# Kernel tuning notes

Measured on AMD Instinct MI355X. Metric: run time of the kernel, lower is better.

Reference implementation:

```python
import jax, jax.numpy as jnp
import numpy as np
import math

B, L, D, P, H, WIN, MAXLEN = 2, 2048, 256, 32, 4, 5, 16384


def setup_inputs() -> dict:
    key = jax.random.key(0)
    ks = iter(jax.random.split(key, 40))
    def w(shape, scale=0.05):
        return jax.random.normal(next(ks), shape, jnp.float32) * scale
    inp = {
        'x': jax.random.normal(next(ks), (B, L, D), jnp.float32),
        'pos_phases': jax.random.normal(next(ks), (MAXLEN, P), jnp.float32) * math.pi,
        # mem1_content_encoder
        'w_content': w((D, D)), 'b_content': jnp.zeros((D,), jnp.float32),
        # head_offset_predictors (stacked over H): Linear(D+P, D//2) -> GELU -> Linear(D//2, P+1)
        'hop_w1': w((H, D // 2, D + P)), 'hop_b1': jnp.zeros((H, D // 2), jnp.float32),
        'hop_w2': w((H, P + 1, D // 2)), 'hop_b2': jnp.zeros((H, P + 1), jnp.float32),
        # content_phase_encoder
        'w_cpe': w((P, D)), 'b_cpe': jnp.zeros((P,), jnp.float32),
        # value_encoder
        'w_val': w((D, D)), 'b_val': jnp.zeros((D,), jnp.float32),
        # kv_context_encoder
        'w_ctx': w((D, D)), 'b_ctx': jnp.zeros((D,), jnp.float32),
        # kv_storage_key: Linear(2D, D) -> GELU -> Linear(D, P)
        'kv_w1': w((D, 2 * D)), 'kv_b1': jnp.zeros((D,), jnp.float32),
        'kv_w2': w((P, D)), 'kv_b2': jnp.zeros((P,), jnp.float32),
        # store_gate: Linear(D, D//2) -> GELU -> Linear(D//2, 1) -> Sigmoid
        'sg_w1': w((D // 2, D)), 'sg_b1': jnp.zeros((D // 2,), jnp.float32),
        'sg_w2': w((1, D // 2)), 'sg_b2': jnp.zeros((1,), jnp.float32),
        # to_out: LayerNorm(D) -> Linear(D, D)
        'ln_g': jnp.ones((D,), jnp.float32), 'ln_b': jnp.zeros((D,), jnp.float32),
        'w_out': w((D, D)), 'b_out': jnp.zeros((D,), jnp.float32),
    }
    return inp


def reference(x, pos_phases, w_content, b_content, hop_w1, hop_b1, hop_w2, hop_b2,
              w_cpe, b_cpe, w_val, b_val, w_ctx, b_ctx, kv_w1, kv_b1, kv_w2, kv_b2,
              sg_w1, sg_b1, sg_w2, sg_b2, ln_g, ln_b, w_out, b_out):
    gelu = lambda t: jax.nn.gelu(t, approximate=False)  # torch exact GELU
    pp = pos_phases[:L]                      # (L,P)
    pos_cos, pos_sin = jnp.cos(pp), jnp.sin(pp)

    # ---- phasor memory 1: position-bound content cumsum ----
    content = x @ w_content.T + b_content    # (B,L,D)
    mem1_cos = jnp.cumsum(pos_cos[None, :, :, None] * content[:, :, None, :], axis=1)  # (B,L,P,D)
    mem1_sin = jnp.cumsum(pos_sin[None, :, :, None] * content[:, :, None, :], axis=1)

    # ---- per-head learned offsets ----
    offset_input = jnp.concatenate([x, jnp.broadcast_to(pp[None], (B, L, P))], axis=-1)  # (B,L,D+P)
    h1 = gelu(jnp.einsum('blf,hgf->bhlg', offset_input, hop_w1) + hop_b1[None, :, None, :])
    off = jnp.einsum('bhlg,hpg->bhlp', h1, hop_w2) + hop_b2[None, :, None, :]  # (B,H,L,P+1)
    center = jnp.tanh(off[..., :P]) * math.pi    # (B,H,L,P)
    ww = jax.nn.sigmoid(off[..., P:]) * 2 + 0.1  # (B,H,L,1)

    head_ret = jnp.zeros((B, H, L, D), x.dtype)
    tot_w = jnp.zeros((B, H, L, 1), x.dtype)
    half = WIN // 2
    for delta in range(-half, half + 1):
        wgt = jnp.exp(-0.5 * delta ** 2 / (ww ** 2 + 1e-6))
        op = center + delta * 0.1
        oc, os = jnp.cos(op), jnp.sin(op)
        qc = pos_cos[None, None] * oc - pos_sin[None, None] * os
        qs = pos_sin[None, None] * oc + pos_cos[None, None] * os
        ret = (jnp.einsum('blpd,bhlp->bhld', mem1_cos, qc)
               + jnp.einsum('blpd,bhlp->bhld', mem1_sin, qs)) / math.sqrt(P)
        head_ret = head_ret + wgt * ret
        tot_w = tot_w + wgt
    multi_head_out = (head_ret / (tot_w + 1e-6)).mean(axis=1)  # (B,L,D)

    # ---- kv phasor memory ----
    key_ph = jnp.tanh(x @ w_cpe.T + b_cpe) * math.pi            # (B,L,P)
    values = x @ w_val.T + b_val                                 # (B,L,D)
    store_gate = jax.nn.sigmoid(gelu(x @ sg_w1.T + sg_b1) @ sg_w2.T + sg_b2)  # (B,L,1)
    ctx = x @ w_ctx.T + b_ctx
    ctx_avg = jnp.cumsum(ctx, axis=1) / jnp.arange(1, L + 1, dtype=x.dtype)[None, :, None]
    storage_in = jnp.concatenate([x, ctx_avg], axis=-1)          # (B,L,2D)
    sp = jnp.tanh(gelu(storage_in @ kv_w1.T + kv_b1) @ kv_w2.T + kv_b2) * math.pi  # (B,L,P)
    gated_v = values * store_gate                                # (B,L,D)
    kv_cos = jnp.cumsum(jnp.cos(sp)[..., None] * gated_v[:, :, None, :], axis=1)  # (B,L,P,D)
    kv_sin = jnp.cumsum(jnp.sin(sp)[..., None] * gated_v[:, :, None, :], axis=1)
    gate_cum = jnp.clip(jnp.cumsum(store_gate, axis=1), 1.0, None)  # (B,L,1)
    kv_ret = (jnp.einsum('blpd,blp->bld', kv_cos, jnp.cos(key_ph))
              + jnp.einsum('blpd,blp->bld', kv_sin, jnp.sin(key_ph)))
    kv_ret = kv_ret / (jnp.sqrt(gate_cum) * math.sqrt(P))

    # ---- output projection ----
    combined = multi_head_out + kv_ret
    mu = combined.mean(-1, keepdims=True)
    var = combined.var(-1, keepdims=True)
    ln = (combined - mu) / jnp.sqrt(var + 1e-5) * ln_g + ln_b
    return x + ln @ w_out.T + b_out
```

## Files before the change

### kernel.cpp

```cpp
#include <hip/hip_runtime.h>
#include <hip/hip_bf16.h>

#define BB 2
#define LL 2048
#define DD 256
#define PP 32
#define PX 64
#define NROW (BB*LL)
#define COLS 1440
#define KIN 288
#define CC 64
#define NC (LL/CC)
#define PI_F 3.14159265358979323846f

typedef __attribute__((ext_vector_type(8))) short bf16x8;
typedef __attribute__((ext_vector_type(4))) float f32x4;

__device__ __forceinline__ float gelu_f(float v){
    return 0.5f*v*(1.0f+erff(v*0.70710678118654752440f));
}
__device__ __forceinline__ float sigm_f(float v){
    return 1.0f/(1.0f+expf(-v));
}
__device__ __forceinline__ short f2b(float v){
    __hip_bfloat16 h = __float2bfloat16(v);
    return *reinterpret_cast<short*>(&h);
}
__device__ __forceinline__ float b2f(unsigned short u){
    unsigned int x = ((unsigned int)u)<<16;
    return __uint_as_float(x);
}

__global__ void kprep(const float* w_content,const float* w_val,const float* w_ctx,
                      const float* w_cpe,const float* sg_w1,const float* hop_w1,
                      const float* b_content,const float* b_val,const float* b_ctx,
                      const float* b_cpe,const float* sg_b1,const float* hop_b1,
                      const float* pos_phases,const float* kv_w1,const float* kv_w2,
                      const float* hop_w2,const float* w_out,const float* x,
                      short* W_catb,float* bias_cat,float* w2mem,
                      short* kvw1b,short* kvw2b,float* hop_w2T,short* w_outb,
                      short* Xb,short* Xin2b){
    int idx = blockIdx.x*256 + threadIdx.x;
    int n1 = COLS*KIN;
    if (idx < n1){
        int row = idx / KIN, k = idx % KIN;
        float v = 0.f;
        if      (row < 256){ if (k<256) v = w_content[row*256+k]; }
        else if (row < 512){ if (k<256) v = w_val[(row-256)*256+k]; }
        else if (row < 768){ if (k<256) v = w_ctx[(row-512)*256+k]; }
        else if (row < 800){ if (k<256) v = w_cpe[(row-768)*256+k]; }
        else if (row < 928){ if (k<256) v = sg_w1[(row-800)*256+k]; }
        else               { v = hop_w1[(row-928)*288 + k]; }
        W_catb[idx] = f2b(v);
        return;
    }
    idx -= n1;
    if (idx < COLS){
        int row = idx; float v = 0.f;
        if      (row < 256) v = b_content[row];
        else if (row < 512) v = b_val[row-256];
        else if (row < 768) v = b_ctx[row-512];
        else if (row < 800) v = b_cpe[row-768];
        else if (row < 928) v = sg_b1[row-800];
        else                v = hop_b1[row-928];
        bias_cat[row] = v;
        return;
    }
    idx -= COLS;
    if (idx < LL*PP){
        int l = idx/PP, p = idx%PP;
        float ph = pos_phases[l*PP+p];
        w2mem[l*PX+p]     = cosf(ph);
        w2mem[l*PX+32+p]  = sinf(ph);
        return;
    }
    idx -= LL*PP;
    if (idx < 256*512){ kvw1b[idx] = f2b(kv_w1[idx]); return; }
    idx -= 256*512;
    if (idx < 32*256){ kvw2b[idx] = f2b(kv_w2[idx]); return; }
    idx -= 32*256;
    if (idx < 128*132){
        int k=idx/132, o=idx%132;
        hop_w2T[idx] = hop_w2[o*128+k];
        return;
    }
    idx -= 128*132;
    if (idx < 256*256){ w_outb[idx] = f2b(w_out[idx]); return; }
    idx -= 256*256;
    if (idx < NROW*KIN){
        int r = idx / KIN, d = idx % KIN;
        float v;
        if (d < 256){ v = x[(size_t)r*DD + d]; Xin2b[(size_t)r*512 + d] = f2b(v); }
        else          v = pos_phases[(r % LL)*PP + (d-256)];
        Xb[idx] = f2b(v);
    }
}

__global__ __launch_bounds__(256) void kA_gemm(const short* Xb,const short* Wb,short* Yb){
    int t=threadIdx.x;
    int wid=t>>6, l=t&63;
    int q=blockIdx.x;
    int ct=q%15, rt=q/15;
    int r0=rt*64 + wid*16;
    int c0=ct*96;
    int lr=l&15, lk=(l>>4)*8;
    const short* ap = Xb + (size_t)(r0+lr)*KIN + lk;
    const short* bp = Wb + (size_t)(c0+lr)*KIN + lk;
    f32x4 acc[6];
    #pragma unroll
    for (int f=0;f<6;f++) acc[f]=(f32x4){0.f,0.f,0.f,0.f};
    for (int ks=0;ks<9;ks++){
        bf16x8 a = *(const bf16x8*)(ap + ks*32);
        #pragma unroll
        for (int f=0;f<6;f++){
            bf16x8 b = *(const bf16x8*)(bp + (size_t)f*16*KIN + ks*32);
            acc[f] = __builtin_amdgcn_mfma_f32_16x16x32_bf16(a,b,acc[f],0,0,0);
        }
    }
    int orow = r0 + (l>>4)*4;
    int ocol = c0 + lr;
    #pragma unroll
    for (int f=0;f<6;f++){
        #pragma unroll
        for (int qq=0;qq<4;qq++){
            Yb[(size_t)(orow+qq)*COLS + ocol + 16*f] = f2b(acc[f][qq]);
        }
    }
}

__global__ __launch_bounds__(256,4) void kA_post(const short* Yb,const float* bias_cat,
        const float* sg_w2,const float* sg_b2,
        const float* hop_w2T,const float* hop_b2,const float* pos_phases,
        short* contentb,short* gatedvb,float* ctx,float* key_ph,
        float* store_gate,float* coef_mem){
    __shared__ float yb[4][1448];
    __shared__ float red[4][32];
    __shared__ float offb[4][136];
    __shared__ float scl[4][4];
    __shared__ float sgvv[4];
    int t=threadIdx.x;
    int r0=blockIdx.x*4;
    {
        const ushort4* Yu4 = (const ushort4*)(Yb) + (size_t)r0*360;
        #pragma unroll
        for (int i=0;i<6;i++){
            int chunk=i*256+t;
            if (chunk<1440){
                int r=chunk/360, c=(chunk%360)*4;
                ushort4 s4 = Yu4[chunk];
                float4 bc = *(const float4*)&bias_cat[c];
                yb[r][c+0]=b2f(s4.x)+bc.x;
                yb[r][c+1]=b2f(s4.y)+bc.y;
                yb[r][c+2]=b2f(s4.z)+bc.z;
                yb[r][c+3]=b2f(s4.w)+bc.w;
            }
        }
    }
    __syncthreads();
    #pragma unroll
    for (int r=0;r<4;r++){
        contentb[(size_t)(r0+r)*DD+t] = f2b(yb[r][t]);
        ctx[(size_t)(r0+r)*DD+t]      = yb[r][512+t];
    }
    #pragma unroll
    for (int j=0;j<8;j++){
        int idx=j*256+t, r=idx>>9, g=idx&511;
        yb[r][928+g] = gelu_f(yb[r][928+g]);
    }
    if (t<128){
        int r=t>>5, j=t&31;
        float s=0.f;
        #pragma unroll
        for (int k=0;k<4;k++){
            int jj=j+32*k;
            s += gelu_f(yb[r][800+jj])*sg_w2[jj];
        }
        red[r][j]=s;
        key_ph[(size_t)(r0+r)*PP+j] = tanhf(yb[r][768+j])*PI_F;
    }
    __syncthreads();
    if (t<128){
        int r=t>>5;
        float s=red[r][t&31];
        #pragma unroll
        for (int off=16;off>=1;off>>=1) s += __shfl_down(s,off,32);
        if ((t&31)==0){
            float g=sigm_f(s+sg_b2[0]);
            sgvv[r]=g;
            store_gate[r0+r]=g;
        }
    }
    for (int sIdx=t; sIdx<528; sIdx+=256){
        int r=sIdx/132, o=sIdx%132, h=o/33;
        const float* yh=&yb[r][928+h*128];
        float a0=0.f,a1=0.f,a2=0.f,a3=0.f;
        #pragma unroll 8
        for (int k=0;k<128;k+=4){
            a0 += hop_w2T[(size_t)(k+0)*132+o]*yh[k+0];
            a1 += hop_w2T[(size_t)(k+1)*132+o]*yh[k+1];
            a2 += hop_w2T[(size_t)(k+2)*132+o]*yh[k+2];
            a3 += hop_w2T[(size_t)(k+3)*132+o]*yh[k+3];
        }
        offb[r][o]=a0+a1+a2+a3+hop_b2[o];
    }
    __syncthreads();
    #pragma unroll
    for (int r=0;r<4;r++) gatedvb[(size_t)(r0+r)*DD+t]=f2b(yb[r][256+t]*sgvv[r]);
    if (t<16){
        int r=t>>2, h=t&3;
        const float c01=0.99500416527802576610f;
        const float c02=0.98006657784124163112f;
        float ww=sigm_f(offb[r][h*33+32])*2.0f+0.1f;
        float iw=1.0f/(ww*ww+1e-6f);
        float w1=expf(-0.5f*iw);
        float w2=expf(-2.0f*iw);
        float tot=1.0f+2.0f*w1+2.0f*w2;
        float Wc =1.0f+2.0f*w1*c01+2.0f*w2*c02;
        scl[r][h]=Wc/((tot+1e-6f)*5.65685424949238019520f*4.0f);
    }
    __syncthreads();
    if (t<128){
        int r=t>>5, p=t&31;
        int l=(r0+r)%LL;
        float ppv=pos_phases[l*PP+p];
        float ca=0.f, sb=0.f;
        #pragma unroll
        for (int h=0;h<4;h++){
            float center=tanhf(offb[r][h*33+p])*PI_F;
            float ang=ppv+center;
            float sc=scl[r][h];
            ca+=sc*cosf(ang);
            sb+=sc*sinf(ang);
        }
        coef_mem[(size_t)(r0+r)*PX+p]=ca;
        coef_mem[(size_t)(r0+r)*PX+32+p]=sb;
    }
}

__global__ void k3a_ctxsum(const float* ctx,float* ctxcs){
    int t=threadIdx.x;
    int bi=blockIdx.x;
    int c=bi%NC, b=bi/NC;
    float s=0.f;
    for (int i=0;i<CC;i++) s += ctx[((size_t)b*LL + c*CC + i)*DD + t];
    ctxcs[(size_t)(b*NC+c)*DD + t] = s;
}
__global__ void k3c_ctxavg(const float* ctx,const float* ctxcs,short* Xin2b){
    int t=threadIdx.x;
    int bi=blockIdx.x;
    int c=bi%NC, b=bi/NC;
    float run=0.f;
    for (int cc=0;cc<c;cc++) run += ctxcs[(size_t)(b*NC+cc)*DD+t];
    for (int i=0;i<CC;i++){
        int l = c*CC+i;
        run += ctx[((size_t)b*LL+l)*DD + t];
        Xin2b[((size_t)b*LL+l)*512 + 256 + t] = f2b(run/(float)(l+1));
    }
}

__global__ __launch_bounds__(256) void kmid(const short* Xin2b,const short* kvw1b,
        const float* kv_b1, short* Hb,
        const float* store_gate,const float* key_ph,float* coefkv){
    __shared__ float sh[2048];
    __shared__ float red[256];
    __shared__ float rsgS[64];
    int t=threadIdx.x;
    if (blockIdx.x < 256){
        int wid=t>>6, l=t&63;
        int q=blockIdx.x;
        int nt=q&3, mt=q>>2;
        int r0=mt*64 + wid*16;
        int c0=nt*64;
        int lr=l&15, lk=(l>>4)*8;
        const short* ap = Xin2b + (size_t)(r0+lr)*512 + lk;
        const short* bp = kvw1b + (size_t)(c0+lr)*512 + lk;
        f32x4 acc[4];
        #pragma unroll
        for (int f=0;f<4;f++) acc[f]=(f32x4){0.f,0.f,0.f,0.f};
        for (int ks=0;ks<16;ks++){
            bf16x8 a = *(const bf16x8*)(ap + ks*32);
            #pragma unroll
            for (int f=0;f<4;f++){
                bf16x8 b = *(const bf16x8*)(bp + (size_t)f*16*512 + ks*32);
                acc[f] = __builtin_amdgcn_mfma_f32_16x16x32_bf16(a,b,acc[f],0,0,0);
            }
        }
        int orow = r0 + (l>>4)*4;
        #pragma unroll
        for (int f=0;f<4;f++){
            int oc = c0 + lr + 16*f;
            float bias = kv_b1[oc];
            #pragma unroll
            for (int qq=0;qq<4;qq++){
                Hb[(size_t)(orow+qq)*256 + oc] = f2b(gelu_f(acc[f][qq]+bias));
            }
        }
        return;
    }
    int q=blockIdx.x-256;
    int c=q&31, b=q>>5;
    int n=(c+1)*CC;
    for (int i=t;i<n;i+=256) sh[i]=store_gate[(size_t)b*LL+i];
    __syncthreads();
    float p=0.f;
    for (int i=t;i<c*CC;i+=256) p+=sh[i];
    red[t]=p;
    __syncthreads();
    for (int off=128;off>=1;off>>=1){
        if (t<off) red[t]+=red[t+off];
        __syncthreads();
    }
    float S0=red[0];
    if (t<64){
        float s=sh[c*CC+t];
        #pragma unroll
        for (int off=1;off<64;off<<=1){
            float v=__shfl_up(s,off);
            if (t>=off) s+=v;
        }
        rsgS[t]=rsqrtf(fmaxf(S0+s,1.0f)*32.0f);
    }
    __syncthreads();
    #pragma unroll
    for (int j=0;j<8;j++){
        int g2=t+j*256;
        int l=g2>>5, pp=g2&31;
        float a=key_ph[((size_t)b*LL + c*CC + l)*PP + pp];
        float rv=rsgS[l];
        coefkv[((size_t)b*LL + c*CC + l)*PX + pp]      = cosf(a)*rv;
        coefkv[((size_t)b*LL + c*CC + l)*PX + 32 + pp] = sinf(a)*rv;
    }
}

__global__ __launch_bounds__(256) void k3d2(const short* Hb,const short* kvw2b,
        const float* kv_b2, float* w2kv){
    int t=threadIdx.x;
    int wid=t>>6, l=t&63;
    int mt=blockIdx.x;
    int r0=mt*64 + wid*16;
    int lr=l&15, lk=(l>>4)*8;
    const short* ap = Hb + (size_t)(r0+lr)*256 + lk;
    const short* bp = kvw2b + (size_t)lr*256 + lk;
    f32x4 acc0=(f32x4){0.f,0.f,0.f,0.f};
    f32x4 acc1=(f32x4){0.f,0.f,0.f,0.f};
    for (int ks=0;ks<8;ks++){
        bf16x8 a  = *(const bf16x8*)(ap + ks*32);
        bf16x8 b0 = *(const bf16x8*)(bp + ks*32);
        bf16x8 b1 = *(const bf16x8*)(bp + (size_t)16*256 + ks*32);
        acc0 = __builtin_amdgcn_mfma_f32_16x16x32_bf16(a,b0,acc0,0,0,0);
        acc1 = __builtin_amdgcn_mfma_f32_16x16x32_bf16(a,b1,acc1,0,0,0);
    }
    int orow=r0+(l>>4)*4;
    #pragma unroll
    for (int f=0;f<2;f++){
        int p = lr + 16*f;
        float bias = kv_b2[p];
        f32x4 av = f? acc1:acc0;
        #pragma unroll
        for (int qq=0;qq<4;qq++){
            float sp=tanhf(av[qq]+bias)*PI_F;
            w2kv[(size_t)(orow+qq)*PX + p]    = cosf(sp);
            w2kv[(size_t)(orow+qq)*PX + 32+p] = sinf(sp);
        }
    }
}

__global__ __launch_bounds__(256) void k4_chunksum(
        const short* valA,const float* w2A,int w2bA,
        const short* valB,const float* w2B,int w2bB,
        float* CS){
    __shared__ float w2s[CC][PX];
    int t=threadIdx.x, q=blockIdx.x;
    int dq=q&3, c=(q>>2)&31, b=(q>>7)&1, inst=q>>8;
    const short* val = inst? valB:valA;
    const float* w2  = inst? w2B:w2A;
    int w2b          = inst? w2bB:w2bA;
    for (int i=0;i<16;i++){
        int idx=i*256+t;
        int l=idx>>6, p=idx&63;
        w2s[l][p]=w2[(size_t)w2b*b + (size_t)(c*CC+l)*PX + p];
    }
    __syncthreads();
    int d=t&63, pg=t>>6;
    float acc[16];
    #pragma unroll
    for (int j=0;j<16;j++) acc[j]=0.f;
    const short* vp = val + ((size_t)b*LL + c*CC)*DD + dq*64 + d;
    for (int l=0;l<CC;l++){
        float v = b2f((unsigned short)vp[(size_t)l*DD]);
        const float4* wr=(const float4*)&w2s[l][pg*16];
        #pragma unroll
        for (int k=0;k<4;k++){
            float4 w=wr[k];
            acc[4*k]   += w.x*v;
            acc[4*k+1] += w.y*v;
            acc[4*k+2] += w.z*v;
            acc[4*k+3] += w.w*v;
        }
    }
    float* cp = CS + (((size_t)(inst*BB+b)*NC + c)*PX + pg*16)*DD + dq*64 + d;
    #pragma unroll
    for (int j=0;j<16;j++) cp[(size_t)j*DD]=acc[j];
}

__global__ void k5_prefix(float* CS){
    int g=blockIdx.x*256+threadIdx.x;
    int d=g&255, p2=(g>>8)&63, b=(g>>14)&1, inst=g>>15;
    size_t base=(((size_t)(inst*BB+b)*NC)*PX+p2)*DD+d;
    float v[NC];
    #pragma unroll
    for (int c=0;c<NC;c++) v[c]=CS[base+(size_t)c*PX*DD];
    float run=0.f;
    #pragma unroll
    for (int c=0;c<NC;c++){
        float tmp=v[c];
        CS[base+(size_t)c*PX*DD]=run;
        run+=tmp;
    }
}

__global__ __launch_bounds__(256) void k6_attn(
        const float* coefA,const float* w2A,int w2bA,const short* valA,float* outA,
        const float* coefB,const float* w2B,int w2bB,const short* valB,float* outB,
        const float* CS){
    __shared__ float coefs[CC][PX+1];
    __shared__ float w2s[CC][PX];
    __shared__ float S[CC][CC+1];
    int t=threadIdx.x, q=blockIdx.x;
    int dq=q&3, qc=(q>>2)&31, b=(q>>7)&1, inst=q>>8;
    const float* coef = inst? coefB:coefA;
    const float* w2   = inst? w2B:w2A;
    int w2b           = inst? w2bB:w2bA;
    const short* val  = inst? valB:valA;
    float* out        = inst? outB:outA;
    int d0 = dq*64;
    for (int i=0;i<16;i++){
        int idx=i*256+t;
        int l=idx>>6, p=idx&63;
        coefs[l][p]=coef[((size_t)b*LL + qc*CC + l)*PX + p];
        w2s[l][p]  =w2[(size_t)w2b*b + (size_t)(qc*CC+l)*PX + p];
    }
    __syncthreads();
    {
        int l=t&63, lpb=(t>>6)*16;
        float cf[PX];
        #pragma unroll
        for (int p=0;p<PX;p++) cf[p]=coefs[l][p];
        for (int qq=0;qq<16;qq++){
            int lp=lpb+qq;
            float s=0.f;
            if (lp<=l){
                const float4* wr=(const float4*)&w2s[lp][0];
                #pragma unroll
                for (int k=0;k<16;k++){
                    float4 w=wr[k];
                    s += w.x*cf[4*k]+w.y*cf[4*k+1]+w.z*cf[4*k+2]+w.w*cf[4*k+3];
                }
            }
            S[l][lp]=s;
        }
    }
    __syncthreads();
    {
        int d=t&63, lq=t>>6;
        float acc[16];
        #pragma unroll
        for (int i=0;i<16;i++) acc[i]=0.f;
        const float* pfx = CS + (((size_t)(inst*BB+b)*NC + qc)*PX)*DD + d0 + d;
        for (int p=0;p<PX;p++){
            float pf = pfx[(size_t)p*DD];
            #pragma unroll
            for (int i=0;i<16;i++) acc[i] += coefs[lq*16+i][p]*pf;
        }
        const short* vptr = val + ((size_t)b*LL + qc*CC)*DD + d0 + d;
        int kmax = lq*16+16;
        for (int lp=0; lp<kmax; lp++){
            float v = b2f((unsigned short)vptr[(size_t)lp*DD]);
            #pragma unroll
            for (int i=0;i<16;i++) acc[i] += S[lq*16+i][lp]*v;
        }
        float* op = out + ((size_t)b*LL + qc*CC + lq*16)*DD + d0 + d;
        #pragma unroll
        for (int i=0;i<16;i++) op[(size_t)i*DD] = acc[i];
    }
}

__global__ __launch_bounds__(256) void k7_final(const float* comb,const float* kvout,
        const float* x,const float* ln_g,const float* ln_b,const short* w_outb,const float* b_out,
        float* out){
    __shared__ float cb[16][260];
    __shared__ short Ab[16][264];
    __shared__ float red[16][32];
    __shared__ float mvm[16][2];
    int t=threadIdx.x, r0=blockIdx.x*16;
    #pragma unroll
    for (int i=0;i<16;i++){
        int idx=i*256+t;
        int r=idx>>8, c=idx&255;
        cb[r][c]=comb[(size_t)(r0+r)*DD+c]+kvout[(size_t)(r0+r)*DD+c];
    }
    __syncthreads();
    {
        int r=t>>4, j=t&15;
        float s=0.f,s2=0.f;
        #pragma unroll
        for (int k=0;k<16;k++){
            float v=cb[r][j+16*k];
            s+=v; s2+=v*v;
        }
        red[r][j]=s; red[r][16+j]=s2;
    }
    __syncthreads();
    if (t<16){
        float s=0.f,s2=0.f;
        #pragma unroll
        for (int j=0;j<16;j++){ s+=red[t][j]; s2+=red[t][16+j]; }
        float mu=s/256.f;
        float var=s2/256.f-mu*mu;
        mvm[t][0]=mu; mvm[t][1]=rsqrtf(var+1e-5f);
    }
    __syncthreads();
    #pragma unroll
    for (int i=0;i<16;i++){
        int idx=i*256+t;
        int r=idx>>8, c=idx&255;
        Ab[r][c]=f2b((cb[r][c]-mvm[r][0])*mvm[r][1]*ln_g[c]+ln_b[c]);
    }
    __syncthreads();
    int wid=t>>6, l=t&63;
    int lr=l&15, lk=(l>>4)*8;
    f32x4 acc[4];
    #pragma unroll
    for (int f=0;f<4;f++) acc[f]=(f32x4){0.f,0.f,0.f,0.f};
    for (int ks=0;ks<8;ks++){
        bf16x8 a = *(const bf16x8*)&Ab[lr][lk+ks*32];
        #pragma unroll
        for (int f=0;f<4;f++){
            bf16x8 bv = *(const bf16x8*)(w_outb + (size_t)(wid*64+f*16+lr)*256 + lk + ks*32);
            acc[f] = __builtin_amdgcn_mfma_f32_16x16x32_bf16(a,bv,acc[f],0,0,0);
        }
    }
    int orow = r0 + (l>>4)*4;
    #pragma unroll
    for (int f=0;f<4;f++){
        int oc = wid*64 + f*16 + lr;
        float bo = b_out[oc];
        #pragma unroll
        for (int qq=0;qq<4;qq++){
            out[(size_t)(orow+qq)*DD + oc] = x[(size_t)(orow+qq)*DD + oc] + acc[f][qq] + bo;
        }
    }
}

extern "C" void kernel_launch(void* const* d_in, const int* in_sizes, int n_in,
                              void* d_out, int out_size, void* d_ws, size_t ws_size,
                              hipStream_t stream){
    (void)in_sizes; (void)n_in; (void)out_size; (void)ws_size;
    const float* x         =(const float*)d_in[0];
    const float* pos_phases=(const float*)d_in[1];
    const float* w_content =(const float*)d_in[2];
    const float* b_content =(const float*)d_in[3];
    const float* hop_w1    =(const float*)d_in[4];
    const float* hop_b1    =(const float*)d_in[5];
    const float* hop_w2    =(const float*)d_in[6];
    const float* hop_b2    =(const float*)d_in[7];
    const float* w_cpe     =(const float*)d_in[8];
    const float* b_cpe     =(const float*)d_in[9];
    const float* w_val     =(const float*)d_in[10];
    const float* b_val     =(const float*)d_in[11];
    const float* w_ctx     =(const float*)d_in[12];
    const float* b_ctx     =(const float*)d_in[13];
    const float* kv_w1     =(const float*)d_in[14];
    const float* kv_b1     =(const float*)d_in[15];
    const float* kv_w2     =(const float*)d_in[16];
    const float* kv_b2     =(const float*)d_in[17];
    const float* sg_w1     =(const float*)d_in[18];
    const float* sg_b1     =(const float*)d_in[19];
    const float* sg_w2     =(const float*)d_in[20];
    const float* sg_b2     =(const float*)d_in[21];
    const float* ln_g      =(const float*)d_in[22];
    const float* ln_b      =(const float*)d_in[23];
    const float* w_out     =(const float*)d_in[24];
    const float* b_out     =(const float*)d_in[25];

    float* ws=(float*)d_ws;
    size_t o=0;
    short* W_catb  =(short*)(ws+o); o+=(size_t)COLS*KIN/2;
    short* Xb      =(short*)(ws+o); o+=(size_t)NROW*KIN/2;
    short* kvw1b   =(short*)(ws+o); o+=(size_t)256*512/2;
    short* kvw2b   =(short*)(ws+o); o+=(size_t)32*256/2;
    short* w_outb  =(short*)(ws+o); o+=(size_t)256*256/2;
    short* Hb      =(short*)(ws+o); o+=(size_t)NROW*256/2;
    short* contentb=(short*)(ws+o); o+=(size_t)NROW*DD/2;
    short* gatedvb =(short*)(ws+o); o+=(size_t)NROW*DD/2;
    float* bias_cat=ws+o; o+=COLS;
    float* hop_w2T =ws+o; o+=(size_t)128*132;
    float* w2mem   =ws+o; o+=(size_t)LL*PX;
    float* ctx     =ws+o; o+=(size_t)NROW*DD;
    float* xin2_kv =ws+o; o+=(size_t)NROW*DD;
    float* key_ph  =ws+o; o+=(size_t)NROW*PP;
    float* store_gate=ws+o; o+=NROW;
    float* coef_mem=ws+o; o+=(size_t)NROW*PX;
    float* coefkv  =ws+o; o+=(size_t)NROW*PX;
    float* w2kv    =ws+o; o+=(size_t)NROW*PX;
    float* ctxcs   =ws+o; o+=(size_t)BB*NC*DD;
    float* CS      =ws+o; o+=(size_t)2*BB*NC*PX*DD;
    short* Yb      =(short*)CS;
    short* Xin2b   =(short*)xin2_kv;
    float* comb  = ctx;
    float* kvout = xin2_kv;

    int prep_total = COLS*KIN + COLS + LL*PP + 256*512 + 32*256 + 128*132 + 256*256 + NROW*KIN;
    kprep<<<(prep_total+255)/256,256,0,stream>>>(
                                 w_content,w_val,w_ctx,w_cpe,sg_w1,hop_w1,
                                 b_content,b_val,b_ctx,b_cpe,sg_b1,hop_b1,
                                 pos_phases,kv_w1,kv_w2,hop_w2,w_out,x,
                                 W_catb,bias_cat,w2mem,kvw1b,kvw2b,hop_w2T,w_outb,Xb,Xin2b);
    kA_gemm<<<960,256,0,stream>>>(Xb,W_catb,Yb);
    kA_post<<<NROW/4,256,0,stream>>>(Yb,bias_cat,sg_w2,sg_b2,hop_w2T,hop_b2,pos_phases,
                                     contentb,gatedvb,ctx,key_ph,store_gate,coef_mem);
    k3a_ctxsum<<<BB*NC,256,0,stream>>>(ctx,ctxcs);
    k3c_ctxavg<<<BB*NC,256,0,stream>>>(ctx,ctxcs,Xin2b);
    kmid<<<256+BB*NC,256,0,stream>>>(Xin2b,kvw1b,kv_b1,Hb,store_gate,key_ph,coefkv);
    k3d2<<<64,256,0,stream>>>(Hb,kvw2b,kv_b2,w2kv);
    k4_chunksum<<<2*BB*NC*4,256,0,stream>>>(contentb,w2mem,0,
                                            gatedvb,w2kv,LL*PX,CS);
    k5_prefix<<<2*BB*PX*DD/256,256,0,stream>>>(CS);
    k6_attn<<<2*BB*NC*4,256,0,stream>>>(coef_mem,w2mem,0,contentb,comb,
                                        coefkv,w2kv,LL*PX,gatedvb,kvout,CS);
    k7_final<<<NROW/16,256,0,stream>>>(comb,kvout,x,ln_g,ln_b,w_outb,b_out,
                                       (float*)d_out);
}
```

Baseline: 147.7 us.

## Reschedule phasor-memory stages into fused multi-role kernels, fuse kv MLP layers

The launch sequence is regrouped so that independent stages share a launch. Memory-1 chunk sums, ctx chunk sums and the kv coefficient pass run in one kernel, and ctx averaging runs alongside the memory-1 prefix scan. Memory-1 attention runs next to a fused two-layer kv storage MLP that keeps the hidden layer in shared memory instead of a global buffer. Prefix sums are now stored in bf16 in a separate buffer, cutting the traffic read by the attention stage but costing precision, and the kv path now runs as its own three-kernel chain.

```diff
diff --git a/kernel.cpp b/kernel.cpp
--- a/kernel.cpp
+++ b/kernel.cpp
@@ -237,148 +237,15 @@
     }
 }
 
-__global__ void k3a_ctxsum(const float* ctx,float* ctxcs){
+__device__ __forceinline__ void k4_body(int q,const short* val,const float* w2,size_t w2b,
+        int instIdx,float* CS,float* smemf){
+    float (*w2s)[PX] = (float(*)[PX])smemf;
     int t=threadIdx.x;
-    int bi=blockIdx.x;
-    int c=bi%NC, b=bi/NC;
-    float s=0.f;
-    for (int i=0;i<CC;i++) s += ctx[((size_t)b*LL + c*CC + i)*DD + t];
-    ctxcs[(size_t)(b*NC+c)*DD + t] = s;
-}
-__global__ void k3c_ctxavg(const float* ctx,const float* ctxcs,short* Xin2b){
-    int t=threadIdx.x;
-    int bi=blockIdx.x;
-    int c=bi%NC, b=bi/NC;
-    float run=0.f;
-    for (int cc=0;cc<c;cc++) run += ctxcs[(size_t)(b*NC+cc)*DD+t];
-    for (int i=0;i<CC;i++){
-        int l = c*CC+i;
-        run += ctx[((size_t)b*LL+l)*DD + t];
-        Xin2b[((size_t)b*LL+l)*512 + 256 + t] = f2b(run/(float)(l+1));
-    }
-}
-
-__global__ __launch_bounds__(256) void kmid(const short* Xin2b,const short* kvw1b,
-        const float* kv_b1, short* Hb,
-        const float* store_gate,const float* key_ph,float* coefkv){
-    __shared__ float sh[2048];
-    __shared__ float red[256];
-    __shared__ float rsgS[64];
-    int t=threadIdx.x;
-    if (blockIdx.x < 256){
-        int wid=t>>6, l=t&63;
-        int q=blockIdx.x;
-        int nt=q&3, mt=q>>2;
-        int r0=mt*64 + wid*16;
-        int c0=nt*64;
-        int lr=l&15, lk=(l>>4)*8;
-        const short* ap = Xin2b + (size_t)(r0+lr)*512 + lk;
-        const short* bp = kvw1b + (size_t)(c0+lr)*512 + lk;
-        f32x4 acc[4];
-        #pragma unroll
-        for (int f=0;f<4;f++) acc[f]=(f32x4){0.f,0.f,0.f,0.f};
-        for (int ks=0;ks<16;ks++){
-            bf16x8 a = *(const bf16x8*)(ap + ks*32);
-            #pragma unroll
-            for (int f=0;f<4;f++){
-                bf16x8 b = *(const bf16x8*)(bp + (size_t)f*16*512 + ks*32);
-                acc[f] = __builtin_amdgcn_mfma_f32_16x16x32_bf16(a,b,acc[f],0,0,0);
-            }
-        }
-        int orow = r0 + (l>>4)*4;
-        #pragma unroll
-        for (int f=0;f<4;f++){
-            int oc = c0 + lr + 16*f;
-            float bias = kv_b1[oc];
-            #pragma unroll
-            for (int qq=0;qq<4;qq++){
-                Hb[(size_t)(orow+qq)*256 + oc] = f2b(gelu_f(acc[f][qq]+bias));
-            }
-        }
-        return;
-    }
-    int q=blockIdx.x-256;
-    int c=q&31, b=q>>5;
-    int n=(c+1)*CC;
-    for (int i=t;i<n;i+=256) sh[i]=store_gate[(size_t)b*LL+i];
-    __syncthreads();
-    float p=0.f;
-    for (int i=t;i<c*CC;i+=256) p+=sh[i];
-    red[t]=p;
-    __syncthreads();
-    for (int off=128;off>=1;off>>=1){
-        if (t<off) red[t]+=red[t+off];
-        __syncthreads();
-    }
-    float S0=red[0];
-    if (t<64){
-        float s=sh[c*CC+t];
-        #pragma unroll
-        for (int off=1;off<64;off<<=1){
-            float v=__shfl_up(s,off);
-            if (t>=off) s+=v;
-        }
-        rsgS[t]=rsqrtf(fmaxf(S0+s,1.0f)*32.0f);
-    }
-    __syncthreads();
-    #pragma unroll
-    for (int j=0;j<8;j++){
-        int g2=t+j*256;
-        int l=g2>>5, pp=g2&31;
-        float a=key_ph[((size_t)b*LL + c*CC + l)*PP + pp];
-        float rv=rsgS[l];
-        coefkv[((size_t)b*LL + c*CC + l)*PX + pp]      = cosf(a)*rv;
-        coefkv[((size_t)b*LL + c*CC + l)*PX + 32 + pp] = sinf(a)*rv;
-    }
-}
-
-__global__ __launch_bounds__(256) void k3d2(const short* Hb,const short* kvw2b,
-        const float* kv_b2, float* w2kv){
-    int t=threadIdx.x;
-    int wid=t>>6, l=t&63;
-    int mt=blockIdx.x;
-    int r0=mt*64 + wid*16;
-    int lr=l&15, lk=(l>>4)*8;
-    const short* ap = Hb + (size_t)(r0+lr)*256 + lk;
-    const short* bp = kvw2b + (size_t)lr*256 + lk;
-    f32x4 acc0=(f32x4){0.f,0.f,0.f,0.f};
-    f32x4 acc1=(f32x4){0.f,0.f,0.f,0.f};
-    for (int ks=0;ks<8;ks++){
-        bf16x8 a  = *(const bf16x8*)(ap + ks*32);
-        bf16x8 b0 = *(const bf16x8*)(bp + ks*32);
-        bf16x8 b1 = *(const bf16x8*)(bp + (size_t)16*256 + ks*32);
-        acc0 = __builtin_amdgcn_mfma_f32_16x16x32_bf16(a,b0,acc0,0,0,0);
-        acc1 = __builtin_amdgcn_mfma_f32_16x16x32_bf16(a,b1,acc1,0,0,0);
-    }
-    int orow=r0+(l>>4)*4;
-    #pragma unroll
-    for (int f=0;f<2;f++){
-        int p = lr + 16*f;
-        float bias = kv_b2[p];
-        f32x4 av = f? acc1:acc0;
-        #pragma unroll
-        for (int qq=0;qq<4;qq++){
-            float sp=tanhf(av[qq]+bias)*PI_F;
-            w2kv[(size_t)(orow+qq)*PX + p]    = cosf(sp);
-            w2kv[(size_t)(orow+qq)*PX + 32+p] = sinf(sp);
-        }
-    }
-}
-
-__global__ __launch_bounds__(256) void k4_chunksum(
-        const short* valA,const float* w2A,int w2bA,
-        const short* valB,const float* w2B,int w2bB,
-        float* CS){
-    __shared__ float w2s[CC][PX];
-    int t=threadIdx.x, q=blockIdx.x;
-    int dq=q&3, c=(q>>2)&31, b=(q>>7)&1, inst=q>>8;
-    const short* val = inst? valB:valA;
-    const float* w2  = inst? w2B:w2A;
-    int w2b          = inst? w2bB:w2bA;
+    int dq=q&3, c=(q>>2)&31, b=q>>7;
     for (int i=0;i<16;i++){
         int idx=i*256+t;
         int l=idx>>6, p=idx&63;
-        w2s[l][p]=w2[(size_t)w2b*b + (size_t)(c*CC+l)*PX + p];
+        w2s[l][p]=w2[w2b*b + (size_t)(c*CC+l)*PX + p];
     }
     __syncthreads();
     int d=t&63, pg=t>>6;
@@ -398,47 +265,38 @@
             acc[4*k+3] += w.w*v;
         }
     }
-    float* cp = CS + (((size_t)(inst*BB+b)*NC + c)*PX + pg*16)*DD + dq*64 + d;
+    float* cp = CS + (((size_t)(instIdx*BB+b)*NC + c)*PX + pg*16)*DD + dq*64 + d;
     #pragma unroll
     for (int j=0;j<16;j++) cp[(size_t)j*DD]=acc[j];
 }
 
-__global__ void k5_prefix(float* CS){
-    int g=blockIdx.x*256+threadIdx.x;
-    int d=g&255, p2=(g>>8)&63, b=(g>>14)&1, inst=g>>15;
-    size_t base=(((size_t)(inst*BB+b)*NC)*PX+p2)*DD+d;
+__device__ __forceinline__ void k5_body(int g,const float* CS,short* PFXb,int instIdx){
+    int d=g&255, p2=(g>>8)&63, b=(g>>14)&1;
+    size_t base=(((size_t)(instIdx*BB+b)*NC)*PX+p2)*DD+d;
     float v[NC];
     #pragma unroll
     for (int c=0;c<NC;c++) v[c]=CS[base+(size_t)c*PX*DD];
     float run=0.f;
     #pragma unroll
     for (int c=0;c<NC;c++){
-        float tmp=v[c];
-        CS[base+(size_t)c*PX*DD]=run;
-        run+=tmp;
-    }
-}
-
-__global__ __launch_bounds__(256) void k6_attn(
-        const float* coefA,const float* w2A,int w2bA,const short* valA,float* outA,
-        const float* coefB,const float* w2B,int w2bB,const short* valB,float* outB,
-        const float* CS){
-    __shared__ float coefs[CC][PX+1];
-    __shared__ float w2s[CC][PX];
-    __shared__ float S[CC][CC+1];
-    int t=threadIdx.x, q=blockIdx.x;
-    int dq=q&3, qc=(q>>2)&31, b=(q>>7)&1, inst=q>>8;
-    const float* coef = inst? coefB:coefA;
-    const float* w2   = inst? w2B:w2A;
-    int w2b           = inst? w2bB:w2bA;
-    const short* val  = inst? valB:valA;
-    float* out        = inst? outB:outA;
+        PFXb[base+(size_t)c*PX*DD]=f2b(run);
+        run+=v[c];
+    }
+}
+
+__device__ __forceinline__ void k6_body(int q,const float* coef,const float* w2,size_t w2b,
+        const short* val,const short* PFXb,int instIdx,float* out,float* smemf){
+    float (*coefs)[PX+1] = (float(*)[PX+1])smemf;
+    float (*w2s)[PX]     = (float(*)[PX])(smemf+64*65);
+    float (*S)[CC+1]     = (float(*)[CC+1])(smemf+64*65+64*64);
+    int t=threadIdx.x;
+    int dq=q&3, qc=(q>>2)&31, b=q>>7;
     int d0 = dq*64;
     for (int i=0;i<16;i++){
         int idx=i*256+t;
         int l=idx>>6, p=idx&63;
         coefs[l][p]=coef[((size_t)b*LL + qc*CC + l)*PX + p];
-        w2s[l][p]  =w2[(size_t)w2b*b + (size_t)(qc*CC+l)*PX + p];
+        w2s[l][p]  =w2[w2b*b + (size_t)(qc*CC+l)*PX + p];
     }
     __syncthreads();
     {
@@ -466,9 +324,9 @@
         float acc[16];
         #pragma unroll
         for (int i=0;i<16;i++) acc[i]=0.f;
-        const float* pfx = CS + (((size_t)(inst*BB+b)*NC + qc)*PX)*DD + d0 + d;
+        const short* pfx = PFXb + (((size_t)(instIdx*BB+b)*NC + qc)*PX)*DD + d0 + d;
         for (int p=0;p<PX;p++){
-            float pf = pfx[(size_t)p*DD];
+            float pf = b2f((unsigned short)pfx[(size_t)p*DD]);
             #pragma unroll
             for (int i=0;i<16;i++) acc[i] += coefs[lq*16+i][p]*pf;
         }
@@ -483,6 +341,154 @@
         #pragma unroll
         for (int i=0;i<16;i++) op[(size_t)i*DD] = acc[i];
     }
+}
+
+__global__ __launch_bounds__(256) void kfat1(const short* contentb,const float* w2mem,float* CS,
+        const float* ctx,float* ctxcs,
+        const float* store_gate,const float* key_ph,float* coefkv){
+    __shared__ float smemf[4160];
+    int t=threadIdx.x, q=blockIdx.x;
+    if (q<512){
+        k4_body(q,contentb,w2mem,0,0,CS,smemf);
+        return;
+    }
+    if (q<576){
+        int bi=q-512;
+        int c=bi%NC, b=bi/NC;
+        float s=0.f;
+        for (int i=0;i<CC;i++) s += ctx[((size_t)b*LL + c*CC + i)*DD + t];
+        ctxcs[(size_t)(b*NC+c)*DD + t] = s;
+        return;
+    }
+    {
+        float* sh  = smemf;
+        float* red = smemf+2048;
+        float* rsgS= smemf+2304;
+        int q3=q-576;
+        int c=q3&31, b=q3>>5;
+        int n=(c+1)*CC;
+        for (int i=t;i<n;i+=256) sh[i]=store_gate[(size_t)b*LL+i];
+        __syncthreads();
+        float p=0.f;
+        for (int i=t;i<c*CC;i+=256) p+=sh[i];
+        red[t]=p;
+        __syncthreads();
+        for (int off=128;off>=1;off>>=1){
+            if (t<off) red[t]+=red[t+off];
+            __syncthreads();
+        }
+        float S0=red[0];
+        if (t<64){
+            float s=sh[c*CC+t];
+            #pragma unroll
+            for (int off=1;off<64;off<<=1){
+                float v=__shfl_up(s,off);
+                if (t>=off) s+=v;
+            }
+            rsgS[t]=rsqrtf(fmaxf(S0+s,1.0f)*32.0f);
+        }
+        __syncthreads();
+        #pragma unroll
+        for (int j=0;j<8;j++){
+            int g2=t+j*256;
+            int l=g2>>5, pp=g2&31;
+            float a=key_ph[((size_t)b*LL + c*CC + l)*PP + pp];
+            float rv=rsgS[l];
+            coefkv[((size_t)b*LL + c*CC + l)*PX + pp]      = cosf(a)*rv;
+            coefkv[((size_t)b*LL + c*CC + l)*PX + 32 + pp] = sinf(a)*rv;
+        }
+    }
+}
+
+__global__ __launch_bounds__(256) void kfat2(const float* ctx,const float* ctxcs,short* Xin2b,
+        const float* CS,short* PFXb){
+    int t=threadIdx.x, q=blockIdx.x;
+    if (q<64){
+        int c=q%NC, b=q/NC;
+        float run=0.f;
+        for (int cc=0;cc<c;cc++) run += ctxcs[(size_t)(b*NC+cc)*DD+t];
+        for (int i=0;i<CC;i++){
+            int l = c*CC+i;
+            run += ctx[((size_t)b*LL+l)*DD + t];
+            Xin2b[((size_t)b*LL+l)*512 + 256 + t] = f2b(run/(float)(l+1));
+        }
+        return;
+    }
+    k5_body((q-64)*256+t,CS,PFXb,0);
+}
+
+__global__ __launch_bounds__(256) void kfat3(
+        const float* coef_mem,const float* w2mem,const short* contentb,
+        const short* PFXb,float* comb,
+        const short* Xin2b,const short* kvw1b,const float* kv_b1,
+        const short* kvw2b,const float* kv_b2,float* w2kv){
+    __shared__ float smemf[12416];
+    int t=threadIdx.x, q=blockIdx.x;
+    if (q<256){
+        k6_body(q,coef_mem,w2mem,0,contentb,PFXb,0,comb,smemf);
+        return;
+    }
+    {
+        short (*Hs)[264] = (short(*)[264])smemf;
+        int mt=q-256;
+        int r0=mt*16;
+        int wid=t>>6, l=t&63;
+        int lr=l&15, lk=(l>>4)*8;
+        const short* ap = Xin2b + (size_t)(r0+lr)*512 + lk;
+        f32x4 acc[4];
+        #pragma unroll
+        for (int f=0;f<4;f++) acc[f]=(f32x4){0.f,0.f,0.f,0.f};
+        for (int ks=0;ks<16;ks++){
+            bf16x8 a = *(const bf16x8*)(ap + ks*32);
+            #pragma unroll
+            for (int f=0;f<4;f++){
+                int c0=wid*64+f*16;
+                bf16x8 b = *(const bf16x8*)(kvw1b + (size_t)(c0+lr)*512 + lk + ks*32);
+                acc[f] = __builtin_amdgcn_mfma_f32_16x16x32_bf16(a,b,acc[f],0,0,0);
+            }
+        }
+        #pragma unroll
+        for (int f=0;f<4;f++){
+            int oc = wid*64 + f*16 + lr;
+            float bias = kv_b1[oc];
+            #pragma unroll
+            for (int qq=0;qq<4;qq++){
+                Hs[(l>>4)*4+qq][oc] = f2b(gelu_f(acc[f][qq]+bias));
+            }
+        }
+        __syncthreads();
+        if (wid<2){
+            const short* bp2 = kvw2b + (size_t)(wid*16+lr)*256 + lk;
+            f32x4 a2=(f32x4){0.f,0.f,0.f,0.f};
+            for (int ks=0;ks<8;ks++){
+                bf16x8 a = *(const bf16x8*)&Hs[lr][lk+ks*32];
+                bf16x8 b = *(const bf16x8*)(bp2 + ks*32);
+                a2 = __builtin_amdgcn_mfma_f32_16x16x32_bf16(a,b,a2,0,0,0);
+            }
+            int p = wid*16 + lr;
+            float bias = kv_b2[p];
+            #pragma unroll
+            for (int qq=0;qq<4;qq++){
+                int orow = r0 + (l>>4)*4 + qq;
+                float sp=tanhf(a2[qq]+bias)*PI_F;
+                w2kv[(size_t)orow*PX + p]    = cosf(sp);
+                w2kv[(size_t)orow*PX + 32+p] = sinf(sp);
+            }
+        }
+    }
+}
+
+__global__ __launch_bounds__(256) void k4B(const short* gatedvb,const float* w2kv,float* CS){
+    __shared__ float smemf[4096];
+    k4_body(blockIdx.x,gatedvb,w2kv,(size_t)LL*PX,1,CS,smemf);
+}
+__global__ void k5B(const float* CS,short* PFXb){
+    k5_body(blockIdx.x*256+threadIdx.x,CS,PFXb,1);
+}
+__global__ __launch_bounds__(256) void k6B(const float* coefkv,const float* w2kv,
+        const short* gatedvb,const short* PFXb,float* kvout){
+    __shared__ float smemf[12416];
+    k6_body(blockIdx.x,coefkv,w2kv,(size_t)LL*PX,gatedvb,PFXb,1,kvout,smemf);
 }
 
 __global__ __launch_bounds__(256) void k7_final(const float* comb,const float* kvout,
@@ -590,9 +596,9 @@
     short* kvw1b   =(short*)(ws+o); o+=(size_t)256*512/2;
     short* kvw2b   =(short*)(ws+o); o+=(size_t)32*256/2;
     short* w_outb  =(short*)(ws+o); o+=(size_t)256*256/2;
-    short* Hb      =(short*)(ws+o); o+=(size_t)NROW*256/2;
     short* contentb=(short*)(ws+o); o+=(size_t)NROW*DD/2;
     short* gatedvb =(short*)(ws+o); o+=(size_t)NROW*DD/2;
+    short* PFXb    =(short*)(ws+o); o+=(size_t)2*BB*NC*PX*DD/2;
     float* bias_cat=ws+o; o+=COLS;
     float* hop_w2T =ws+o; o+=(size_t)128*132;
     float* w2mem   =ws+o; o+=(size_t)LL*PX;
@@ -619,15 +625,13 @@
     kA_gemm<<<960,256,0,stream>>>(Xb,W_catb,Yb);
     kA_post<<<NROW/4,256,0,stream>>>(Yb,bias_cat,sg_w2,sg_b2,hop_w2T,hop_b2,pos_phases,
                                      contentb,gatedvb,ctx,key_ph,store_gate,coef_mem);
-    k3a_ctxsum<<<BB*NC,256,0,stream>>>(ctx,ctxcs);
-    k3c_ctxavg<<<BB*NC,256,0,stream>>>(ctx,ctxcs,Xin2b);
-    kmid<<<256+BB*NC,256,0,stream>>>(Xin2b,kvw1b,kv_b1,Hb,store_gate,key_ph,coefkv);
-    k3d2<<<64,256,0,stream>>>(Hb,kvw2b,kv_b2,w2kv);
-    k4_chunksum<<<2*BB*NC*4,256,0,stream>>>(contentb,w2mem,0,
-                                            gatedvb,w2kv,LL*PX,CS);
-    k5_prefix<<<2*BB*PX*DD/256,256,0,stream>>>(CS);
-    k6_attn<<<2*BB*NC*4,256,0,stream>>>(coef_mem,w2mem,0,contentb,comb,
-                                        coefkv,w2kv,LL*PX,gatedvb,kvout,CS);
+    kfat1<<<640,256,0,stream>>>(contentb,w2mem,CS,ctx,ctxcs,store_gate,key_ph,coefkv);
+    kfat2<<<192,256,0,stream>>>(ctx,ctxcs,Xin2b,CS,PFXb);
+    kfat3<<<512,256,0,stream>>>(coef_mem,w2mem,contentb,PFXb,comb,
+                                Xin2b,kvw1b,kv_b1,kvw2b,kv_b2,w2kv);
+    k4B<<<512,256,0,stream>>>(gatedvb,w2kv,CS);
+    k5B<<<128,256,0,stream>>>(CS,PFXb);
+    k6B<<<256,256,0,stream>>>(coefkv,w2kv,gatedvb,PFXb,kvout);
     k7_final<<<NROW/16,256,0,stream>>>(comb,kvout,x,ln_g,ln_b,w_outb,b_out,
                                        (float*)d_out);
 }
```

Measured after the change: 159.6 us. +8.0%, slower.
